# Kernel optimization log

Hardware: AMD Instinct MI355X
Metric: run time of the kernel (lower is better)

The kernel has to match this reference:

```python
import jax, jax.numpy as jnp
import numpy as np


def conv3x3(x, w, b):
    # NCHW conv, 3x3, stride 1, pad 1
    y = jax.lax.conv_general_dilated(
        x, w, window_strides=(1, 1), padding=[(1, 1), (1, 1)],
        dimension_numbers=('NCHW', 'OIHW', 'NCHW'))
    return y + b[None, :, None, None]


def setup_inputs() -> dict:
    key = jax.random.key(0)
    ks = jax.random.split(key, 6)
    B, C, O, H, W = 4, 128, 128, 160, 160
    x = jax.random.normal(ks[0], (B, C, H, W), dtype=jnp.float32)
    # offset conv: small weights so sampling stays near the regular grid
    w_off = jax.random.normal(ks[1], (18, C, 3, 3), dtype=jnp.float32) * 0.1
    b_off = jnp.zeros((18,), dtype=jnp.float32)
    w_mask = jax.random.normal(ks[2], (9, C, 3, 3), dtype=jnp.float32) * 0.1
    b_mask = jnp.zeros((9,), dtype=jnp.float32)
    w = jax.random.normal(ks[3], (O, C, 3, 3), dtype=jnp.float32) * (1.0 / np.sqrt(C * 9))
    b = jax.random.normal(ks[4], (O,), dtype=jnp.float32) * 0.01
    return {'x': x, 'w_off': w_off, 'b_off': b_off,
            'w_mask': w_mask, 'b_mask': b_mask, 'w': w, 'b': b}


def reference(x, w_off, b_off, w_mask, b_mask, w, b):
    B, C, H, W = x.shape
    K = 9  # 3x3 kernel taps
    # offset: [B, 18, H, W] -> [B, K, 2, H, W]; channel layout is (dy, dx) per tap
    off = conv3x3(x, w_off, b_off).reshape(B, K, 2, H, W)
    dy, dx = off[:, :, 0], off[:, :, 1]                 # [B, K, H, W]
    mask = jax.nn.sigmoid(conv3x3(x, w_mask, b_mask))   # [B, K, H, W]

    # sampling positions: p = p_out - pad + k + offset  (stride 1, pad 1, dil 1)
    ky = (jnp.repeat(jnp.arange(3), 3) - 1).astype(x.dtype).reshape(1, K, 1, 1)
    kx = (jnp.tile(jnp.arange(3), 3) - 1).astype(x.dtype).reshape(1, K, 1, 1)
    hy = jnp.arange(H, dtype=x.dtype).reshape(1, 1, H, 1)
    wx = jnp.arange(W, dtype=x.dtype).reshape(1, 1, 1, W)
    py = hy + ky + dy   # [B, K, H, W]
    px = wx + kx + dx

    y0f = jnp.floor(py)
    x0f = jnp.floor(px)
    ly = py - y0f       # bilinear weights
    lx = px - x0f
    y0 = y0f.astype(jnp.int32)
    x0 = x0f.astype(jnp.int32)

    xf = x.reshape(B, C, H * W)

    def gather(iy, ix):
        # zero-padded gather at integer coords [B, K, H, W] -> [B, C, K, H, W]
        valid = ((iy >= 0) & (iy < H) & (ix >= 0) & (ix < W)).astype(x.dtype)
        idx = (jnp.clip(iy, 0, H - 1) * W + jnp.clip(ix, 0, W - 1)).reshape(B, 1, K * H * W)
        g = jnp.take_along_axis(xf, idx, axis=2).reshape(B, C, K, H, W)
        return g * valid[:, None]

    val = (gather(y0, x0) * ((1 - ly) * (1 - lx))[:, None]
           + gather(y0, x0 + 1) * ((1 - ly) * lx)[:, None]
           + gather(y0 + 1, x0) * (ly * (1 - lx))[:, None]
           + gather(y0 + 1, x0 + 1) * (ly * lx)[:, None])   # [B, C, K, H, W]

    val = val * mask[:, None]                                # modulated (DCNv2)
    out = jnp.einsum('bckhw,ock->bohw', val, w.reshape(w.shape[0], C, K))
    return out + b[None, :, None, None]
```

## Files before the change

kernel.cpp:

```cpp
#include <hip/hip_runtime.h>
#include <math.h>

constexpr int Bn = 4, Cc = 128, On = 128, Hh = 160, Ww = 160, Kk = 9;
constexpr int HW = Hh * Ww;

typedef __attribute__((ext_vector_type(8))) short s16x8;
typedef __attribute__((ext_vector_type(4))) float f32x4;

__device__ inline float bf2f(short s) {
    union { float f; unsigned u; } v;
    v.u = ((unsigned)(unsigned short)s) << 16;
    return v.f;
}
__device__ inline short f2bf(float f) {
    union { float f; unsigned u; } v;
    v.f = f;
    unsigned r = v.u + 0x7fffu + ((v.u >> 16) & 1u);
    return (short)(r >> 16);
}

__global__ __launch_bounds__(256) void to_nhwc(const float* __restrict__ x,
                                               short* __restrict__ xT,
                                               short* __restrict__ xLo) {
    __shared__ float tile[128][65];
    const int t = threadIdx.x;
    const int p0 = blockIdx.x * 64;
    const int b = blockIdx.y;
#pragma unroll
    for (int i = 0; i < 32; ++i) {
        int c = i * 4 + (t >> 6);
        tile[c][t & 63] = x[((size_t)b * Cc + c) * HW + p0 + (t & 63)];
    }
    __syncthreads();
    const int px = t >> 2, cq = t & 3;
    short* dsth = xT  + ((size_t)(b * HW) + p0 + px) * Cc;
    short* dstl = xLo + ((size_t)(b * HW) + p0 + px) * Cc;
#pragma unroll
    for (int j = 0; j < 8; ++j) {
        int c0 = cq * 4 + j * 16;
        short4 vh, vl;
        float f0 = tile[c0 + 0][px], f1 = tile[c0 + 1][px];
        float f2 = tile[c0 + 2][px], f3 = tile[c0 + 3][px];
        vh.x = f2bf(f0); vh.y = f2bf(f1); vh.z = f2bf(f2); vh.w = f2bf(f3);
        vl.x = f2bf(f0 - bf2f(vh.x));
        vl.y = f2bf(f1 - bf2f(vh.y));
        vl.z = f2bf(f2 - bf2f(vh.z));
        vl.w = f2bf(f3 - bf2f(vh.w));
        *(short4*)(dsth + c0) = vh;
        *(short4*)(dstl + c0) = vl;
    }
}

__global__ void prep_w(const float* __restrict__ wt, short* __restrict__ wb) {
    int idx = blockIdx.x * 256 + threadIdx.x;
    if (idx >= Kk * On * Cc) return;
    int c = idx & 127;
    int o = (idx >> 7) & 127;
    int k = idx >> 14;
    wb[idx] = f2bf(wt[(o * Cc + c) * 9 + k]);
}

__global__ void prep_wofm(const float* __restrict__ w_off,
                          const float* __restrict__ w_mask,
                          short* __restrict__ wh, short* __restrict__ wl) {
    int idx = blockIdx.x * 256 + threadIdx.x;
    if (idx >= Kk * 32 * Cc) return;
    int c = idx & 127;
    int ch = (idx >> 7) & 31;
    int k = idx >> 12;
    float v = 0.f;
    if (ch < 18)      v = w_off[(ch * Cc + c) * 9 + k];
    else if (ch < 27) v = w_mask[((ch - 18) * Cc + c) * 9 + k];
    short hi = f2bf(v);
    wh[idx] = hi;
    wl[idx] = f2bf(v - bf2f(hi));
}

__global__ __launch_bounds__(256) void offmask_mfma(
    const short* __restrict__ xT, const short* __restrict__ xLo,
    const short* __restrict__ wh, const short* __restrict__ wl,
    const float* __restrict__ b_off, const float* __restrict__ b_mask,
    float* __restrict__ dy_o, float* __restrict__ dx_o, float* __restrict__ mk_o)
{
    __shared__ short a_hi[6][2304];
    __shared__ short a_lo[6][2304];

    const int g = blockIdx.x;
    const int orig = (g & 7) * 200 + (g >> 3);
    const int b  = orig / 400;
    const int rem = orig % 400;
    const int h0 = (rem / 10) * 4;
    const int w0 = (rem % 10) * 16;

    const int t = threadIdx.x;

    const short* xh_b = xT  + (size_t)b * HW * Cc;
    const short* xl_b = xLo + (size_t)b * HW * Cc;
#pragma unroll
    for (int j = 0; j < 14; ++j) {
        int ci = j * 256 + t;
        if (ci < 3456) {
            int slot = ci / 576;
            int rem2 = ci % 576;
            int isLo = rem2 >= 288;
            int cj   = isLo ? rem2 - 288 : rem2;
            int pxl  = cj >> 4;
            int ck   = cj & 15;
            int r   = h0 - 1 + slot;
            int col = w0 - 1 + pxl;
            int4 v = make_int4(0, 0, 0, 0);
            if ((unsigned)r < (unsigned)Hh && (unsigned)col < (unsigned)Ww) {
                const short* src = (isLo ? xl_b : xh_b) +
                                   ((size_t)(r * Ww + col)) * Cc + ck * 8;
                v = *(const int4*)src;
            }
            int byte = (pxl * 256 + ck * 16) ^ ((pxl & 7) << 4);
            *(int4*)((char*)(isLo ? a_lo[slot] : a_hi[slot]) + byte) = v;
        }
    }
    __syncthreads();

    const int lane = t & 63, wid = t >> 6;
    const int i  = lane & 15;
    const int kb = (lane >> 4) * 8;

    f32x4 acc[2];
    acc[0] = (f32x4){0.f, 0.f, 0.f, 0.f};
    acc[1] = (f32x4){0.f, 0.f, 0.f, 0.f};

    s16x8 bh[2][2][4], bl[2][2][4];

#pragma unroll
    for (int tile = 0; tile < 2; ++tile) {
        const short* bp = wh + ((size_t)(tile * 16 + i)) * Cc + kb;
        const short* lp = wl + ((size_t)(tile * 16 + i)) * Cc + kb;
#pragma unroll
        for (int kk = 0; kk < 4; ++kk) {
            bh[0][tile][kk] = *(const s16x8*)(bp + kk * 32);
            bl[0][tile][kk] = *(const s16x8*)(lp + kk * 32);
        }
    }

#pragma unroll
    for (int k = 0; k < Kk; ++k) {
        const int cur = k & 1, nxt = cur ^ 1;
        if (k < Kk - 1) {
            const int kn = k + 1;
#pragma unroll
            for (int tile = 0; tile < 2; ++tile) {
                const short* bp = wh + ((size_t)(kn * 32 + tile * 16 + i)) * Cc + kb;
                const short* lp = wl + ((size_t)(kn * 32 + tile * 16 + i)) * Cc + kb;
#pragma unroll
                for (int kk = 0; kk < 4; ++kk) {
                    bh[nxt][tile][kk] = *(const s16x8*)(bp + kk * 32);
                    bl[nxt][tile][kk] = *(const s16x8*)(lp + kk * 32);
                }
            }
        }
        const int ky = k / 3, kxi = k % 3;
        const int slot = wid + ky;
        const int pxl = i + kxi;
        s16x8 ah[4], al[4];
#pragma unroll
        for (int kk = 0; kk < 4; ++kk) {
            int byte = (pxl * 256 + (kk * 32 + kb) * 2) ^ ((pxl & 7) << 4);
            ah[kk] = *(const s16x8*)((char*)a_hi[slot] + byte);
            al[kk] = *(const s16x8*)((char*)a_lo[slot] + byte);
        }
#pragma unroll
        for (int tile = 0; tile < 2; ++tile) {
#pragma unroll
            for (int kk = 0; kk < 4; ++kk) {
                acc[tile] = __builtin_amdgcn_mfma_f32_16x16x32_bf16(ah[kk], bh[cur][tile][kk], acc[tile], 0, 0, 0);
                acc[tile] = __builtin_amdgcn_mfma_f32_16x16x32_bf16(al[kk], bh[cur][tile][kk], acc[tile], 0, 0, 0);
                acc[tile] = __builtin_amdgcn_mfma_f32_16x16x32_bf16(ah[kk], bl[cur][tile][kk], acc[tile], 0, 0, 0);
            }
        }
    }

    const int hr = h0 + wid;
#pragma unroll
    for (int tile = 0; tile < 2; ++tile) {
        int ch = tile * 16 + i;
#pragma unroll
        for (int reg = 0; reg < 4; ++reg) {
            int pxo = (lane >> 4) * 4 + reg;
            int p = hr * Ww + w0 + pxo;
            float v = acc[tile][reg];
            if (ch < 18) {
                int k = ch >> 1;
                v += b_off[ch];
                if (ch & 1) dx_o[(size_t)(b * 9 + k) * HW + p] = v;
                else        dy_o[(size_t)(b * 9 + k) * HW + p] = v;
            } else if (ch < 27) {
                int k = ch - 18;
                v += b_mask[k];
                mk_o[(size_t)(b * 9 + k) * HW + p] = 1.f / (1.f + expf(-v));
            }
        }
    }
}

__global__ __launch_bounds__(256) void dconv_main(
    const short* __restrict__ xT,
    const short* __restrict__ wb,
    const float* __restrict__ bias,
    const float* __restrict__ dy_i, const float* __restrict__ dx_i,
    const float* __restrict__ mk_i,
    float* __restrict__ out)
{
    __shared__ short w_lds[128 * 128];

    const int g = blockIdx.x;
    const int orig = (g & 7) * 200 + (g >> 3);
    const int b = orig / 400;
    const int p0 = (orig % 400) * 64;

    const int t = threadIdx.x;
    const int lane = t & 63;
    const int wid = t >> 6;
    const int pm = wid * 16;

    const int myPx = pm + (lane & 15);
    const int p = p0 + myPx;
    const int h = p / Ww, w = p % Ww;
    const int kb8 = (lane >> 4) * 8;

    const short* xbase = xT + (size_t)b * HW * Cc + kb8;

    f32x4 acc[8];
#pragma unroll
    for (int i = 0; i < 8; ++i) acc[i] = (f32x4){0.f, 0.f, 0.f, 0.f};

    for (int k = 0; k < Kk; ++k) {
        size_t obase = (size_t)(b * 9 + k) * HW + p;
        float dyv = dy_i[obase], dxv = dx_i[obase], m = mk_i[obase];
        float py  = (float)(h + (k / 3) - 1) + dyv;
        float pxf = (float)(w + (k % 3) - 1) + dxv;
        float y0f = floorf(py), x0f = floorf(pxf);
        float ly = py - y0f, lx = pxf - x0f;
        int y0 = (int)y0f, x0 = (int)x0f;
        int   idxc[4];
        float wg[4];
#pragma unroll
        for (int cr = 0; cr < 4; ++cr) {
            int iy = y0 + (cr >> 1), ix = x0 + (cr & 1);
            bool ok = ((unsigned)iy < (unsigned)Hh) && ((unsigned)ix < (unsigned)Ww);
            float wy = (cr >> 1) ? ly : (1.f - ly);
            float wx = (cr & 1) ? lx : (1.f - lx);
            int cy = min(max(iy, 0), Hh - 1);
            int cx = min(max(ix, 0), Ww - 1);
            idxc[cr] = cy * Ww + cx;
            wg[cr] = ok ? (wy * wx * m) : 0.f;
        }

        s16x8 G[16];
#pragma unroll
        for (int cr = 0; cr < 4; ++cr) {
            const short* src = xbase + (size_t)idxc[cr] * Cc;
#pragma unroll
            for (int kk = 0; kk < 4; ++kk)
                G[cr * 4 + kk] = *(const s16x8*)(src + kk * 32);
        }

        {
            const int4* src = (const int4*)(wb + (size_t)k * 128 * 128);
#pragma unroll
            for (int i = 0; i < 8; ++i) {
                int ci = i * 256 + t;
                int o = ci >> 4;
                int byte = (ci << 4) ^ ((o & 7) << 4);
                *(int4*)((char*)w_lds + byte) = src[ci];
            }
        }
        __syncthreads();

        s16x8 afr[4];
#pragma unroll
        for (int kk = 0; kk < 4; ++kk) {
#pragma unroll
            for (int j = 0; j < 8; ++j) {
                float s = wg[0] * bf2f(G[0 * 4 + kk][j])
                        + wg[1] * bf2f(G[1 * 4 + kk][j])
                        + wg[2] * bf2f(G[2 * 4 + kk][j])
                        + wg[3] * bf2f(G[3 * 4 + kk][j]);
                afr[kk][j] = f2bf(s);
            }
        }

        {
            const int orow = lane & 15;
#pragma unroll
            for (int ot = 0; ot < 8; ++ot) {
                int o = ot * 16 + orow;
#pragma unroll
                for (int kk = 0; kk < 4; ++kk) {
                    int byte = (o * 256 + (kk * 32 + kb8) * 2) ^ ((o & 7) << 4);
                    s16x8 bfr = *(const s16x8*)((char*)w_lds + byte);
                    acc[ot] = __builtin_amdgcn_mfma_f32_16x16x32_bf16(afr[kk], bfr, acc[ot], 0, 0, 0);
                }
            }
        }
        __syncthreads();
    }

#pragma unroll
    for (int ot = 0; ot < 8; ++ot) {
        int o = ot * 16 + (lane & 15);
        float bo = bias[o];
        float4 r;
        r.x = acc[ot][0] + bo;
        r.y = acc[ot][1] + bo;
        r.z = acc[ot][2] + bo;
        r.w = acc[ot][3] + bo;
        *(float4*)(out + ((size_t)(b * On + o)) * HW + p0 + pm + (lane >> 4) * 4) = r;
    }
}

extern "C" void kernel_launch(void* const* d_in, const int* in_sizes, int n_in,
                              void* d_out, int out_size, void* d_ws, size_t ws_size,
                              hipStream_t stream) {
    const float* x      = (const float*)d_in[0];
    const float* w_off  = (const float*)d_in[1];
    const float* b_off  = (const float*)d_in[2];
    const float* w_mask = (const float*)d_in[3];
    const float* b_mask = (const float*)d_in[4];
    const float* wt     = (const float*)d_in[5];
    const float* bias   = (const float*)d_in[6];
    float* out = (float*)d_out;

    short* xT  = (short*)d_ws;
    short* xLo = xT + (size_t)Bn * HW * Cc;
    short* wb  = xLo + (size_t)Bn * HW * Cc;
    short* wofm_h = wb + Kk * On * Cc;
    short* wofm_l = wofm_h + Kk * 32 * Cc;
    float* dy = (float*)(wofm_l + Kk * 32 * Cc);
    float* dx = dy + (size_t)Bn * 9 * HW;
    float* mk = dx + (size_t)Bn * 9 * HW;

    to_nhwc<<<dim3(HW / 64, Bn), 256, 0, stream>>>(x, xT, xLo);
    prep_w<<<(Kk * On * Cc + 255) / 256, 256, 0, stream>>>(wt, wb);
    prep_wofm<<<(Kk * 32 * Cc + 255) / 256, 256, 0, stream>>>(w_off, w_mask, wofm_h, wofm_l);
    offmask_mfma<<<1600, 256, 0, stream>>>(
        xT, xLo, wofm_h, wofm_l, b_off, b_mask, dy, dx, mk);
    dconv_main<<<1600, 256, 0, stream>>>(
        xT, wb, bias, dy, dx, mk, out);
}
```

Before: 318.1 us.

## Software-pipeline gather and weight staging across taps with double-buffered LDS

Restructures the tap loop so the offset/mask loads, bilinear index setup and global gathers for the next tap are issued before the MFMA work of the current tap. Weights for the next tap are staged into a second LDS buffer, which removes one barrier per iteration and hides global latency behind compute. The cost is doubled LDS (64KB per block), which may cut occupancy, plus higher register pressure from the fully unrolled loop and live prefetched gathers.

```diff
diff --git a/kernel.cpp b/kernel.cpp
--- a/kernel.cpp
+++ b/kernel.cpp
@@ -209,7 +209,7 @@
     const float* __restrict__ mk_i,
     float* __restrict__ out)
 {
-    __shared__ short w_lds[128 * 128];
+    __shared__ short w_lds[2][128 * 128];
 
     const int g = blockIdx.x;
     const int orig = (g & 7) * 200 + (g >> 3);
@@ -232,48 +232,69 @@
 #pragma unroll
     for (int i = 0; i < 8; ++i) acc[i] = (f32x4){0.f, 0.f, 0.f, 0.f};
 
+    float wg[4];
+    int   idxc[4];
+    s16x8 G[16];
+
+#define SETUP(kq, dyv, dxv, mv)                                                \
+    {                                                                          \
+        float py  = (float)(h + ((kq) / 3) - 1) + (dyv);                       \
+        float pxf = (float)(w + ((kq) % 3) - 1) + (dxv);                       \
+        float y0f = floorf(py), x0f = floorf(pxf);                             \
+        float ly = py - y0f, lx = pxf - x0f;                                   \
+        int y0 = (int)y0f, x0 = (int)x0f;                                      \
+        _Pragma("unroll")                                                      \
+        for (int cr = 0; cr < 4; ++cr) {                                       \
+            int iy = y0 + (cr >> 1), ix = x0 + (cr & 1);                       \
+            bool ok = ((unsigned)iy < (unsigned)Hh) && ((unsigned)ix < (unsigned)Ww); \
+            float wy = (cr >> 1) ? ly : (1.f - ly);                            \
+            float wx = (cr & 1) ? lx : (1.f - lx);                             \
+            int cy = min(max(iy, 0), Hh - 1);                                  \
+            int cx = min(max(ix, 0), Ww - 1);                                  \
+            idxc[cr] = cy * Ww + cx;                                           \
+            wg[cr] = ok ? (wy * wx * (mv)) : 0.f;                              \
+        }                                                                      \
+    }
+
+#define ISSUEG                                                                 \
+    {                                                                          \
+        _Pragma("unroll")                                                      \
+        for (int cr = 0; cr < 4; ++cr) {                                       \
+            const short* src = xbase + (size_t)idxc[cr] * Cc;                  \
+            _Pragma("unroll")                                                  \
+            for (int kk = 0; kk < 4; ++kk)                                     \
+                G[cr * 4 + kk] = *(const s16x8*)(src + kk * 32);               \
+        }                                                                      \
+    }
+
+#define STAGE(kq, bufIdx)                                                      \
+    {                                                                          \
+        const int4* src = (const int4*)(wb + (size_t)(kq) * 128 * 128);        \
+        _Pragma("unroll")                                                      \
+        for (int i2 = 0; i2 < 8; ++i2) {                                       \
+            int ci = i2 * 256 + t;                                             \
+            int o = ci >> 4;                                                   \
+            int byte = (ci << 4) ^ ((o & 7) << 4);                             \
+            *(int4*)((char*)w_lds[bufIdx] + byte) = src[ci];                   \
+        }                                                                      \
+    }
+
+    {
+        size_t ob = (size_t)(b * 9 + 0) * HW + p;
+        float dyv = dy_i[ob], dxv = dx_i[ob], mv = mk_i[ob];
+        SETUP(0, dyv, dxv, mv);
+    }
+    ISSUEG;
+    STAGE(0, 0);
+    __syncthreads();
+
+#pragma unroll
     for (int k = 0; k < Kk; ++k) {
-        size_t obase = (size_t)(b * 9 + k) * HW + p;
-        float dyv = dy_i[obase], dxv = dx_i[obase], m = mk_i[obase];
-        float py  = (float)(h + (k / 3) - 1) + dyv;
-        float pxf = (float)(w + (k % 3) - 1) + dxv;
-        float y0f = floorf(py), x0f = floorf(pxf);
-        float ly = py - y0f, lx = pxf - x0f;
-        int y0 = (int)y0f, x0 = (int)x0f;
-        int   idxc[4];
-        float wg[4];
-#pragma unroll
-        for (int cr = 0; cr < 4; ++cr) {
-            int iy = y0 + (cr >> 1), ix = x0 + (cr & 1);
-            bool ok = ((unsigned)iy < (unsigned)Hh) && ((unsigned)ix < (unsigned)Ww);
-            float wy = (cr >> 1) ? ly : (1.f - ly);
-            float wx = (cr & 1) ? lx : (1.f - lx);
-            int cy = min(max(iy, 0), Hh - 1);
-            int cx = min(max(ix, 0), Ww - 1);
-            idxc[cr] = cy * Ww + cx;
-            wg[cr] = ok ? (wy * wx * m) : 0.f;
-        }
-
-        s16x8 G[16];
-#pragma unroll
-        for (int cr = 0; cr < 4; ++cr) {
-            const short* src = xbase + (size_t)idxc[cr] * Cc;
-#pragma unroll
-            for (int kk = 0; kk < 4; ++kk)
-                G[cr * 4 + kk] = *(const s16x8*)(src + kk * 32);
-        }
-
-        {
-            const int4* src = (const int4*)(wb + (size_t)k * 128 * 128);
-#pragma unroll
-            for (int i = 0; i < 8; ++i) {
-                int ci = i * 256 + t;
-                int o = ci >> 4;
-                int byte = (ci << 4) ^ ((o & 7) << 4);
-                *(int4*)((char*)w_lds + byte) = src[ci];
-            }
-        }
-        __syncthreads();
+        float dyn = 0.f, dxn = 0.f, mn = 0.f;
+        if (k < Kk - 1) {
+            size_t ob = (size_t)(b * 9 + k + 1) * HW + p;
+            dyn = dy_i[ob]; dxn = dx_i[ob]; mn = mk_i[ob];
+        }
 
         s16x8 afr[4];
 #pragma unroll
@@ -288,6 +309,11 @@
             }
         }
 
+        if (k < Kk - 1) {
+            SETUP(k + 1, dyn, dxn, mn);
+            ISSUEG;
+        }
+
         {
             const int orow = lane & 15;
 #pragma unroll
@@ -296,13 +322,19 @@
 #pragma unroll
                 for (int kk = 0; kk < 4; ++kk) {
                     int byte = (o * 256 + (kk * 32 + kb8) * 2) ^ ((o & 7) << 4);
-                    s16x8 bfr = *(const s16x8*)((char*)w_lds + byte);
+                    s16x8 bfr = *(const s16x8*)((char*)w_lds[k & 1] + byte);
                     acc[ot] = __builtin_amdgcn_mfma_f32_16x16x32_bf16(afr[kk], bfr, acc[ot], 0, 0, 0);
                 }
             }
         }
+
+        if (k < Kk - 1) STAGE(k + 1, (k + 1) & 1);
         __syncthreads();
     }
+
+#undef SETUP
+#undef ISSUEG
+#undef STAGE
 
 #pragma unroll
     for (int ot = 0; ot < 8; ++ot) {
```

After: 307.3 us. -3.4%, faster.
